# Optimization experiments

Measured on AMD Instinct MI355X. Metric: run time of the kernel, lower is better.

The kernel has to match this reference:

```python
import jax, jax.numpy as jnp
import numpy as np

# GridEncoder(d=3, L=16, F=2, b=2, N_min=16, log2_hashmap_size=19, gridtype='hash'), bound=1
D = 3
L = 16
F = 2
N_MIN = 16
PLS = 2.0            # per_level_scale b
LOG2_T = 19
BOUND = 1.0
N_CORNERS = 2 ** D
# fast_hash primes from the CUDA kernel (first D entries)
PRIMES = (np.uint32(1), np.uint32(2654435761), np.uint32(805459861))


def _offsets_and_res():
    """Replicates the Python offsets loop and the kernel's per-level resolution."""
    S = np.log2(PLS)
    offs = [0]
    res = []
    off = 0
    for l in range(L):
        scale = np.exp2(l * S) * N_MIN - 1.0      # kernel: scale = exp2f(level*S)*H - 1
        res.append(int(np.ceil(scale)) + 1)       # kernel: resolution = ceil(scale)+1
        N_l = int(np.ceil(N_MIN * PLS ** l))
        T = min(2 ** LOG2_T, (N_l + 1) ** D)
        off += T
        offs.append(off)
    return offs, res

OFFSETS, RES = _offsets_and_res()  # OFFSETS[-1] == 7131219


def setup_inputs() -> dict:
    k1, k2 = jax.random.split(jax.random.key(0))
    inputs = jax.random.uniform(k1, (1_000_000, D), jnp.float32, -1.0, 1.0)
    embeddings = jax.random.uniform(k2, (OFFSETS[-1], F), jnp.float32, -1e-4, 1e-4)
    return {"inputs": inputs, "embeddings": embeddings}


def _encode(inputs, embeddings):
    # normalize to [0,1] as in GridEncoder.forward
    x = (inputs + BOUND) / (2 * BOUND)            # [B, D]
    B = x.shape[0]
    S = np.log2(PLS)
    outs = []
    for l in range(L):  # fixed small level count -> Python loop is fine
        hmap = OFFSETS[l + 1] - OFFSETS[l]
        emb = embeddings[OFFSETS[l]:OFFSETS[l + 1]]   # static slice [hmap, F]
        resolution = RES[l]
        scale = np.float32(np.exp2(l * S) * N_MIN - 1.0)
        pos = x * scale + 0.5
        pg = jnp.floor(pos)
        frac = pos - pg                               # [B, D] in [0,1)
        pg = pg.astype(jnp.uint32)
        use_hash = (resolution + 1) ** D > hmap       # static per level
        acc = jnp.zeros((B, F), x.dtype)
        for corner in range(N_CORNERS):               # 8 corners, multilinear interp
            w = jnp.ones((B,), x.dtype)
            idx = jnp.zeros((B,), jnp.uint32)
            stride = 1
            for d in range(D):
                bit = (corner >> d) & 1
                g = pg[:, d] + np.uint32(bit)         # corner grid coord (uint32)
                w = w * (frac[:, d] if bit else (1.0 - frac[:, d]))
                if use_hash:
                    idx = idx ^ (g * PRIMES[d])       # uint32 wraparound == fast_hash
                else:
                    idx = idx + g * np.uint32(stride)
                    stride *= (resolution + 1)
            idx = (idx % np.uint32(hmap)).astype(jnp.int32)
            acc = acc + w[:, None] * emb[idx]         # gather [B, F]
        outs.append(acc)
    return jnp.concatenate(outs, axis=-1)             # [B, L*F], level-major like permute+reshape


def reference(inputs, embeddings):
    return _encode(inputs, embeddings)
```

## Files before the change

### kernel.cpp

```cpp
#include <hip/hip_runtime.h>
#include <cstdint>


static constexpr uint32_t kOff[17] = {
    0u, 4913u, 40850u, 315475u, 839763u, 1364051u, 1888339u, 2412627u,
    2936915u, 3461203u, 3985491u, 4509779u, 5034067u, 5558355u, 6082643u,
    6606931u, 7131219u};

static constexpr uint32_t P1 = 2654435761u;
static constexpr uint32_t P2 = 805459861u;

typedef float f4a8 __attribute__((ext_vector_type(4), aligned(8)));
typedef float v2f __attribute__((ext_vector_type(2)));
typedef float v4f __attribute__((ext_vector_type(4)));

__device__ __forceinline__ float2 ntload2(const float2* p) {
  v2f t = __builtin_nontemporal_load((const v2f*)p);
  return make_float2(t[0], t[1]);
}
__device__ __forceinline__ void ntstore2(float2* p, float a, float b) {
  v2f t;
  t[0] = a;
  t[1] = b;
  __builtin_nontemporal_store(t, (v2f*)p);
}
__device__ __forceinline__ void ntstore4(float4* p, float a, float b, float c,
                                         float d) {
  v4f t;
  t[0] = a;
  t[1] = b;
  t[2] = c;
  t[3] = d;
  __builtin_nontemporal_store(t, (v4f*)p);
}

__device__ __forceinline__ float to_unit(float v) {
  return __fmul_rn(__fadd_rn(v, 1.0f), 0.5f);
}

__device__ __forceinline__ void pos_decomp_rt(float x0, float x1, float x2,
                                              float scale, uint32_t& i0,
                                              uint32_t& i1, uint32_t& i2,
                                              float& f0, float& f1, float& f2) {
  float p0 = __fadd_rn(__fmul_rn(x0, scale), 0.5f);
  float p1 = __fadd_rn(__fmul_rn(x1, scale), 0.5f);
  float p2 = __fadd_rn(__fmul_rn(x2, scale), 0.5f);
  float g0 = floorf(p0), g1 = floorf(p1), g2 = floorf(p2);
  f0 = __fsub_rn(p0, g0);
  f1 = __fsub_rn(p1, g1);
  f2 = __fsub_rn(p2, g2);
  i0 = (uint32_t)g0;
  i1 = (uint32_t)g1;
  i2 = (uint32_t)g2;
}

__device__ __forceinline__ void hashed_accum_rt(float x0, float x1, float x2,
                                                float scale,
                                                const float2* __restrict__ t2,
                                                float& A0, float& A1) {
  constexpr uint32_t mask = 0x7FFFFu;
  uint32_t i0, i1, i2;
  float f0, f1, f2;
  pos_decomp_rt(x0, x1, x2, scale, i0, i1, i2, f0, f1, f2);

  const float w0l = __fsub_rn(1.0f, f0), w0h = f0;
  const float w1v[2] = {__fsub_rn(1.0f, f1), f1};
  const float w2v[2] = {__fsub_rn(1.0f, f2), f2};
  uint32_t h1v[2], h2v[2];
  h1v[0] = i1 * P1;
  h1v[1] = h1v[0] + P1;
  h2v[0] = i2 * P2;
  h2v[1] = h2v[0] + P2;

  const bool odd = (i0 & 1u) != 0u;
  float acc0 = A0, acc1 = A1;
#pragma unroll
  for (int b2 = 0; b2 < 2; ++b2) {
#pragma unroll
    for (int b1 = 0; b1 < 2; ++b1) {
      const uint32_t ex = h1v[b1] ^ h2v[b2];
      const uint32_t ilo = (i0 ^ ex) & mask;
      const f4a8 v = *(const f4a8*)(t2 + (ilo & ~1u));
      const bool hs = (ilo & 1u) != 0u;
      float eL0 = hs ? v.z : v.x;
      float eL1 = hs ? v.w : v.y;
      float eH0 = hs ? v.x : v.z;
      float eH1 = hs ? v.y : v.w;
      if (odd) {
        const uint32_t ihi = ((i0 + 1u) ^ ex) & mask;
        const float2 e = t2[ihi];
        eH0 = e.x;
        eH1 = e.y;
      }
      const float wl = __fmul_rn(__fmul_rn(w0l, w1v[b1]), w2v[b2]);
      const float wh = __fmul_rn(__fmul_rn(w0h, w1v[b1]), w2v[b2]);
      acc0 = __fadd_rn(acc0, __fmul_rn(wl, eL0));
      acc1 = __fadd_rn(acc1, __fmul_rn(wl, eL1));
      acc0 = __fadd_rn(acc0, __fmul_rn(wh, eH0));
      acc1 = __fadd_rn(acc1, __fmul_rn(wh, eH1));
    }
  }
  A0 = acc0;
  A1 = acc1;
}

template <int LV>
__device__ __forceinline__ void dense_accum(float x0, float x1, float x2,
                                            const float* __restrict__ embf,
                                            float& A0, float& A1) {
  static_assert(LV < 3, "");
  constexpr uint32_t res = 16u << LV;
  constexpr uint32_t off = kOff[LV];
  constexpr uint32_t s1 = res + 1u, s2 = s1 * s1;
  constexpr float scale = (float)res - 1.0f;
  uint32_t i0, i1, i2;
  float f0, f1, f2;
  pos_decomp_rt(x0, x1, x2, scale, i0, i1, i2, f0, f1, f2);

  const float w0l = __fsub_rn(1.0f, f0), w0h = f0;
  const float w1v[2] = {__fsub_rn(1.0f, f1), f1};
  const float w2v[2] = {__fsub_rn(1.0f, f2), f2};
  const uint32_t base = i0 + i1 * s1 + i2 * s2;
  const float2* t2 = (const float2*)embf + off;

  float acc0 = A0, acc1 = A1;
#pragma unroll
  for (int b2 = 0; b2 < 2; ++b2) {
#pragma unroll
    for (int b1 = 0; b1 < 2; ++b1) {
      const uint32_t idx = base + (b1 ? s1 : 0u) + (b2 ? s2 : 0u);
      const f4a8 v = *(const f4a8*)(t2 + idx);
      const float wl = __fmul_rn(__fmul_rn(w0l, w1v[b1]), w2v[b2]);
      const float wh = __fmul_rn(__fmul_rn(w0h, w1v[b1]), w2v[b2]);
      acc0 = __fadd_rn(acc0, __fmul_rn(wl, v.x));
      acc1 = __fadd_rn(acc1, __fmul_rn(wl, v.y));
      acc0 = __fadd_rn(acc0, __fmul_rn(wh, v.z));
      acc1 = __fadd_rn(acc1, __fmul_rn(wh, v.w));
    }
  }
  A0 = acc0;
  A1 = acc1;
}


__global__ __launch_bounds__(256) void mega_kernel(
    const float* __restrict__ in, const float* __restrict__ embf,
    float2* __restrict__ ws, int B, int NB) {
  const int zone = blockIdx.x / NB;
  const int q = (blockIdx.x - zone * NB) * 256 + threadIdx.x;
  const int p0 = q << 1;
  if (p0 >= B) return;
  const bool hasB = (p0 + 1) < B;

  float xA0, xA1, xA2, xB0 = 0.f, xB1 = 0.f, xB2 = 0.f;
  if (hasB) {
    const float2* in2 = (const float2*)in;
    const size_t b3 = (size_t)q * 3;
    const float2 u0 = ntload2(in2 + b3);
    const float2 u1 = ntload2(in2 + b3 + 1);
    const float2 u2 = ntload2(in2 + b3 + 2);
    xA0 = to_unit(u0.x);
    xA1 = to_unit(u0.y);
    xA2 = to_unit(u1.x);
    xB0 = to_unit(u1.y);
    xB1 = to_unit(u2.x);
    xB2 = to_unit(u2.y);
  } else {
    xA0 = to_unit(in[(size_t)p0 * 3 + 0]);
    xA1 = to_unit(in[(size_t)p0 * 3 + 1]);
    xA2 = to_unit(in[(size_t)p0 * 3 + 2]);
  }
  const bool pair4 = hasB && ((B & 1) == 0);

  if (zone == 0) {
    float a0, a1, b0, b1;
#define DO_DENSE(LV)                                              \
  a0 = a1 = b0 = b1 = 0.0f;                                       \
  dense_accum<LV>(xA0, xA1, xA2, embf, a0, a1);                   \
  if (hasB) dense_accum<LV>(xB0, xB1, xB2, embf, b0, b1);         \
  {                                                               \
    float2* wsl = ws + (size_t)LV * B;                            \
    if (pair4)                                                    \
      ntstore4((float4*)(wsl + p0), a0, a1, b0, b1);              \
    else {                                                        \
      ntstore2(wsl + p0, a0, a1);                                 \
      if (hasB) ntstore2(wsl + p0 + 1, b0, b1);                   \
    }                                                             \
  }
    DO_DENSE(0)
    DO_DENSE(1)
    DO_DENSE(2)
#undef DO_DENSE
  } else {
    const int level = zone + 2;
    const float scale = (float)(int)((16u << level) - 1u);
    const float2* t2 =
        (const float2*)embf + (315475u + (uint32_t)(level - 3) * 524288u);
    float2* wsl = ws + (size_t)level * B;

    float a0 = 0.0f, a1 = 0.0f;
    hashed_accum_rt(xA0, xA1, xA2, scale, t2, a0, a1);
    if (pair4) {
      float b0 = 0.0f, b1 = 0.0f;
      hashed_accum_rt(xB0, xB1, xB2, scale, t2, b0, b1);
      ntstore4((float4*)(wsl + p0), a0, a1, b0, b1);
    } else {
      ntstore2(wsl + p0, a0, a1);
      if (hasB) {
        float b0 = 0.0f, b1 = 0.0f;
        hashed_accum_rt(xB0, xB1, xB2, scale, t2, b0, b1);
        ntstore2(wsl + p0 + 1, b0, b1);
      }
    }
  }
}


__global__ __launch_bounds__(256) void transpose_kernel(
    const float2* __restrict__ ws, float4* __restrict__ out4, size_t n4,
    int B) {
  const size_t g = (size_t)blockIdx.x * 256 + threadIdx.x;
  if (g >= n4) return;
  const int p = (int)(g >> 3);
  const int j = (int)(g & 7);
  const float2 e0 = ntload2(ws + (size_t)(2 * j) * B + p);
  const float2 e1 = ntload2(ws + (size_t)(2 * j + 1) * B + p);
  ntstore4(out4 + g, e0.x, e0.y, e1.x, e1.y);
}


template <int LV>
__device__ __forceinline__ void any_accum(float x0, float x1, float x2,
                                          const float* __restrict__ embf,
                                          float& A0, float& A1) {
  if constexpr (LV < 3) {
    dense_accum<LV>(x0, x1, x2, embf, A0, A1);
  } else {
    constexpr float scale = (float)(16u << LV) - 1.0f;
    const float2* t2 = (const float2*)embf + kOff[LV];
    hashed_accum_rt(x0, x1, x2, scale, t2, A0, A1);
  }
}

template <int LBASE>
__global__ __launch_bounds__(256) void grid_enc_kernel(
    const float* __restrict__ in, const float* __restrict__ embf,
    float* __restrict__ out, int B) {
  const int p = blockIdx.x * 256 + threadIdx.x;
  if (p >= B) return;
  const float x0 = to_unit(in[(size_t)p * 3 + 0]);
  const float x1 = to_unit(in[(size_t)p * 3 + 1]);
  const float x2 = to_unit(in[(size_t)p * 3 + 2]);

  float a[16];
#pragma unroll
  for (int i = 0; i < 16; ++i) a[i] = 0.0f;

  any_accum<LBASE + 0>(x0, x1, x2, embf, a[0], a[1]);
  any_accum<LBASE + 1>(x0, x1, x2, embf, a[2], a[3]);
  any_accum<LBASE + 2>(x0, x1, x2, embf, a[4], a[5]);
  any_accum<LBASE + 3>(x0, x1, x2, embf, a[6], a[7]);
  any_accum<LBASE + 4>(x0, x1, x2, embf, a[8], a[9]);
  any_accum<LBASE + 5>(x0, x1, x2, embf, a[10], a[11]);
  any_accum<LBASE + 6>(x0, x1, x2, embf, a[12], a[13]);
  any_accum<LBASE + 7>(x0, x1, x2, embf, a[14], a[15]);

  float4* __restrict__ o = (float4*)(out + (size_t)p * 32 + LBASE * 2);
  o[0] = make_float4(a[0], a[1], a[2], a[3]);
  o[1] = make_float4(a[4], a[5], a[6], a[7]);
  o[2] = make_float4(a[8], a[9], a[10], a[11]);
  o[3] = make_float4(a[12], a[13], a[14], a[15]);
}

extern "C" void kernel_launch(void* const* d_in, const int* in_sizes, int n_in,
                              void* d_out, int out_size, void* d_ws,
                              size_t ws_size, hipStream_t stream) {
  const float* in = (const float*)d_in[0];
  const float* emb = (const float*)d_in[1];
  float* out = (float*)d_out;
  const int B = in_sizes[0] / 3;
  const size_t ws_needed = (size_t)16 * (size_t)B * sizeof(float2);

  if (ws_size >= ws_needed) {
    float2* ws = (float2*)d_ws;
    const int NB = ((B + 1) / 2 + 255) / 256;
    mega_kernel<<<NB * 14, 256, 0, stream>>>(in, emb, ws, B, NB);
    const size_t n4 = (size_t)B * 8;
    const int tb = (int)((n4 + 255) / 256);
    transpose_kernel<<<tb, 256, 0, stream>>>(ws, (float4*)out, n4, B);
  } else {
    const int blocksP = (B + 255) / 256;
    grid_enc_kernel<0><<<blocksP, 256, 0, stream>>>(in, emb, out, B);
    grid_enc_kernel<8><<<blocksP, 256, 0, stream>>>(in, emb, out, B);
  }
}
```

Before: 708.0 us.

## Move dense levels into transpose kernel and stage output through LDS

The three dense levels move out of the hashed mega kernel's zone 0 into the final kernel, which now also computes them per point. The mega kernel launches 13 zones covering only the hashed levels 3-15. The old transpose kernel is replaced by a final kernel that reads the 13 hashed results from workspace and transposes all 32 outputs per point through shared memory. The stores then go out coalesced. This cuts the workspace write and read traffic for three levels and gives the output a coalesced write pattern, at the cost of a heavier final kernel and extra register pressure from the 32-float array.

```diff
diff --git a/kernel.cpp b/kernel.cpp
--- a/kernel.cpp
+++ b/kernel.cpp
@@ -172,60 +172,76 @@
   }
   const bool pair4 = hasB && ((B & 1) == 0);
 
-  if (zone == 0) {
-    float a0, a1, b0, b1;
-#define DO_DENSE(LV)                                              \
-  a0 = a1 = b0 = b1 = 0.0f;                                       \
-  dense_accum<LV>(xA0, xA1, xA2, embf, a0, a1);                   \
-  if (hasB) dense_accum<LV>(xB0, xB1, xB2, embf, b0, b1);         \
-  {                                                               \
-    float2* wsl = ws + (size_t)LV * B;                            \
-    if (pair4)                                                    \
-      ntstore4((float4*)(wsl + p0), a0, a1, b0, b1);              \
-    else {                                                        \
-      ntstore2(wsl + p0, a0, a1);                                 \
-      if (hasB) ntstore2(wsl + p0 + 1, b0, b1);                   \
-    }                                                             \
-  }
-    DO_DENSE(0)
-    DO_DENSE(1)
-    DO_DENSE(2)
-#undef DO_DENSE
+  const int level = zone + 3;
+  const float scale = (float)(int)((16u << level) - 1u);
+  const float2* t2 =
+      (const float2*)embf + (315475u + (uint32_t)(level - 3) * 524288u);
+  float2* wsl = ws + (size_t)level * B;
+
+  float a0 = 0.0f, a1 = 0.0f;
+  hashed_accum_rt(xA0, xA1, xA2, scale, t2, a0, a1);
+  if (pair4) {
+    float b0 = 0.0f, b1 = 0.0f;
+    hashed_accum_rt(xB0, xB1, xB2, scale, t2, b0, b1);
+    ntstore4((float4*)(wsl + p0), a0, a1, b0, b1);
   } else {
-    const int level = zone + 2;
-    const float scale = (float)(int)((16u << level) - 1u);
-    const float2* t2 =
-        (const float2*)embf + (315475u + (uint32_t)(level - 3) * 524288u);
-    float2* wsl = ws + (size_t)level * B;
-
-    float a0 = 0.0f, a1 = 0.0f;
-    hashed_accum_rt(xA0, xA1, xA2, scale, t2, a0, a1);
-    if (pair4) {
+    ntstore2(wsl + p0, a0, a1);
+    if (hasB) {
       float b0 = 0.0f, b1 = 0.0f;
       hashed_accum_rt(xB0, xB1, xB2, scale, t2, b0, b1);
-      ntstore4((float4*)(wsl + p0), a0, a1, b0, b1);
-    } else {
-      ntstore2(wsl + p0, a0, a1);
-      if (hasB) {
-        float b0 = 0.0f, b1 = 0.0f;
-        hashed_accum_rt(xB0, xB1, xB2, scale, t2, b0, b1);
-        ntstore2(wsl + p0 + 1, b0, b1);
-      }
-    }
-  }
-}
-
-
-__global__ __launch_bounds__(256) void transpose_kernel(
-    const float2* __restrict__ ws, float4* __restrict__ out4, size_t n4,
-    int B) {
-  const size_t g = (size_t)blockIdx.x * 256 + threadIdx.x;
-  if (g >= n4) return;
-  const int p = (int)(g >> 3);
-  const int j = (int)(g & 7);
-  const float2 e0 = ntload2(ws + (size_t)(2 * j) * B + p);
-  const float2 e1 = ntload2(ws + (size_t)(2 * j + 1) * B + p);
-  ntstore4(out4 + g, e0.x, e0.y, e1.x, e1.y);
+      ntstore2(wsl + p0 + 1, b0, b1);
+    }
+  }
+}
+
+
+__global__ __launch_bounds__(256) void final_kernel(
+    const float* __restrict__ in, const float* __restrict__ embf,
+    const float2* __restrict__ ws, float4* __restrict__ out4, int B) {
+  __shared__ float4 lds[4 * 257];
+  const int tid = (int)threadIdx.x;
+  const int p = blockIdx.x * 256 + tid;
+
+  float a[32];
+#pragma unroll
+  for (int i = 0; i < 32; ++i) a[i] = 0.0f;
+
+  if (p < B) {
+    const float x0 = to_unit(in[(size_t)p * 3 + 0]);
+    const float x1 = to_unit(in[(size_t)p * 3 + 1]);
+    const float x2 = to_unit(in[(size_t)p * 3 + 2]);
+    dense_accum<0>(x0, x1, x2, embf, a[0], a[1]);
+    dense_accum<1>(x0, x1, x2, embf, a[2], a[3]);
+    dense_accum<2>(x0, x1, x2, embf, a[4], a[5]);
+#pragma unroll
+    for (int l = 3; l < 16; ++l) {
+      const float2 e = ws[(size_t)l * B + p];
+      a[2 * l] = e.x;
+      a[2 * l + 1] = e.y;
+    }
+  }
+
+  const size_t gbase = (size_t)blockIdx.x * 2048;
+  const size_t lim = (size_t)B * 8;
+#pragma unroll
+  for (int half = 0; half < 2; ++half) {
+    if (half) __syncthreads();
+#pragma unroll
+    for (int w = 0; w < 4; ++w) {
+      const int qd = half * 4 + w;
+      lds[w * 257 + tid] =
+          make_float4(a[4 * qd], a[4 * qd + 1], a[4 * qd + 2], a[4 * qd + 3]);
+    }
+    __syncthreads();
+#pragma unroll
+    for (int k = 0; k < 4; ++k) {
+      const int gl = k * 256 + tid;
+      const int pt = gl >> 2;
+      const int qw = gl & 3;
+      const size_t g = gbase + (size_t)pt * 8 + (size_t)(half * 4 + qw);
+      if (g < lim) out4[g] = lds[qw * 257 + pt];
+    }
+  }
 }
 
 
@@ -284,10 +300,9 @@
   if (ws_size >= ws_needed) {
     float2* ws = (float2*)d_ws;
     const int NB = ((B + 1) / 2 + 255) / 256;
-    mega_kernel<<<NB * 14, 256, 0, stream>>>(in, emb, ws, B, NB);
-    const size_t n4 = (size_t)B * 8;
-    const int tb = (int)((n4 + 255) / 256);
-    transpose_kernel<<<tb, 256, 0, stream>>>(ws, (float4*)out, n4, B);
+    mega_kernel<<<NB * 13, 256, 0, stream>>>(in, emb, ws, B, NB);
+    const int blocksP = (B + 255) / 256;
+    final_kernel<<<blocksP, 256, 0, stream>>>(in, emb, ws, (float4*)out, B);
   } else {
     const int blocksP = (B + 255) / 256;
     grid_enc_kernel<0><<<blocksP, 256, 0, stream>>>(in, emb, out, B);
```

Result: slower. 769.2 us (+8.6%).
